# Kernel optimization log

Measured on AMD Instinct MI355X. Metric: run time of the kernel, lower is better.

The kernel has to match this reference:

```python
import jax, jax.numpy as jnp
import numpy as np

B, H, S, D = 4, 16, 2048, 128

def setup_inputs() -> dict:
    key = jax.random.key(0)
    kq, kk, kv = jax.random.split(key, 3)
    query = jax.random.normal(kq, (B, H, S, D), dtype=jnp.float32)
    k = jax.random.normal(kk, (B, H, S, D), dtype=jnp.float32)
    value = jax.random.normal(kv, (B, H, S, D), dtype=jnp.float32)
    attn_mask = jnp.zeros((B, H, S, S), dtype=jnp.float32)
    return {"query": query, "key": k, "value": value, "attn_mask": attn_mask}

def reference(query, key, value, attn_mask):
    # scores: [B,H,S,S]
    scale = 1.0 / jnp.sqrt(jnp.asarray(query.shape[-1], query.dtype))
    scores = jnp.einsum('bhqd,bhkd->bhqk', query, key) * scale + attn_mask
    attn = jax.nn.softmax(scores, axis=-1)
    out = jnp.einsum('bhqk,bhkd->bhqd', attn, value)
    return out
```

## Files before the change

kernel.cpp:

```cpp
#include <hip/hip_runtime.h>

#define SDIM 2048
#define DDIM 128
#define NBH  64
#define BR   128
#define BC   64
#define PSTRIDE 72

using bf16x8 = __attribute__((ext_vector_type(8))) short;
using f32x4  = __attribute__((ext_vector_type(4))) float;

typedef const __attribute__((address_space(1))) void* gvp;
typedef __attribute__((address_space(3))) void* lvp;

static __device__ __forceinline__ short f2bf(float x) {
    unsigned u = __float_as_uint(x);
    u += 0x7fff + ((u >> 16) & 1);
    return (short)(u >> 16);
}
static __device__ __forceinline__ unsigned pack2(float a, float b) {
    return ((unsigned)(unsigned short)f2bf(a)) |
           (((unsigned)(unsigned short)f2bf(b)) << 16);
}

__global__ __launch_bounds__(256) void kconv_kernel(const float* __restrict__ K,
                                                    unsigned short* __restrict__ Kc)
{
    size_t i = ((size_t)blockIdx.x * 256 + threadIdx.x) * 4;
    float4 v = *(const float4*)(K + i);
    uint2 o;
    o.x = pack2(v.x, v.y);
    o.y = pack2(v.z, v.w);
    *(uint2*)(Kc + i) = o;
}

__global__ __launch_bounds__(256) void vtrans_kernel(const float* __restrict__ V,
                                                     unsigned short* __restrict__ Vt)
{
    __shared__ float t[32][33];
    const int bh = blockIdx.z;
    const int s0 = blockIdx.x * 32;
    const int d0 = blockIdx.y * 32;
    const int x = threadIdx.x & 31;
    const int y = threadIdx.x >> 5;
    const float* Vb = V + (size_t)bh * SDIM * DDIM;
    unsigned short* Vtb = Vt + (size_t)bh * SDIM * DDIM;
#pragma unroll
    for (int i = 0; i < 4; ++i) {
        int r = y + i * 8;
        t[r][x] = Vb[(size_t)(s0 + r) * DDIM + d0 + x];
    }
    __syncthreads();
#pragma unroll
    for (int i = 0; i < 4; ++i) {
        int r = y + i * 8;
        Vtb[(size_t)(d0 + r) * SDIM + s0 + x] = (unsigned short)f2bf(t[x][r]);
    }
}

static __device__ __forceinline__ void stage_K(const unsigned short* __restrict__ Kb,
                                               char* __restrict__ Kdst,
                                               int k0, int wave, int quad, int n16)
{
#pragma unroll
    for (int j = 0; j < 4; ++j) {
        const int row = wave * 16 + j * 4 + quad;
        const int src = (n16 * 16) ^ ((row & 7) << 4);
        const char* gp = (const char*)(Kb + (size_t)(k0 + row) * DDIM) + src;
        __builtin_amdgcn_global_load_lds((gvp)gp, (lvp)(Kdst + wave * 4096 + j * 1024), 16, 0, 0);
    }
}
static __device__ __forceinline__ void stage_V(const unsigned short* __restrict__ Vb,
                                               char* __restrict__ Vdst,
                                               int k0, int wave, int lane)
{
#pragma unroll
    for (int j = 0; j < 4; ++j) {
        const int row = wave * 32 + j * 8 + (lane >> 3);
        const int src = ((lane & 7) * 16) ^ ((row & 7) << 4);
        const char* gp = (const char*)(Vb + (size_t)row * SDIM + k0) + src;
        __builtin_amdgcn_global_load_lds((gvp)gp, (lvp)(Vdst + wave * 4096 + j * 1024), 16, 0, 0);
    }
}

static __device__ __forceinline__ void load_mask(const float* __restrict__ Mb,
                                                 int q0, int wave, int quad, int n16,
                                                 int kcol, float (&mk)[2][4][4])
{
#pragma unroll
    for (int rt = 0; rt < 2; ++rt) {
        const int rowb = q0 + wave * 32 + rt * 16 + quad * 4;
        const float* mpb = Mb + (size_t)rowb * SDIM + kcol + n16;
#pragma unroll
        for (int ct = 0; ct < 4; ++ct)
#pragma unroll
            for (int r = 0; r < 4; ++r)
                mk[rt][ct][r] = mpb[(size_t)r * SDIM + ct * 16];
    }
}

static __device__ __forceinline__ void softmax_update(
    f32x4 (&s)[2][4], f32x4 (&acc)[2][8], float (&mrow)[2][4], float (&lrow)[2][4])
{
    float mx[2][4];
#pragma unroll
    for (int rt = 0; rt < 2; ++rt)
#pragma unroll
        for (int r = 0; r < 4; ++r)
            mx[rt][r] = fmaxf(fmaxf(s[rt][0][r], s[rt][1][r]),
                              fmaxf(s[rt][2][r], s[rt][3][r]));
#pragma unroll
    for (int st = 1; st <= 8; st <<= 1)
#pragma unroll
        for (int rt = 0; rt < 2; ++rt)
#pragma unroll
            for (int r = 0; r < 4; ++r)
                mx[rt][r] = fmaxf(mx[rt][r], __shfl_xor(mx[rt][r], st));

    int anynew = 0;
#pragma unroll
    for (int rt = 0; rt < 2; ++rt)
#pragma unroll
        for (int r = 0; r < 4; ++r)
            anynew |= (mx[rt][r] > mrow[rt][r]) ? 1 : 0;
    if (__ballot(anynew) != 0ull) {
#pragma unroll
        for (int rt = 0; rt < 2; ++rt)
#pragma unroll
            for (int r = 0; r < 4; ++r) {
                float mnew = fmaxf(mrow[rt][r], mx[rt][r]);
                float al = exp2f((mrow[rt][r] - mnew) * 1.44269504f);
                mrow[rt][r] = mnew;
                lrow[rt][r] *= al;
#pragma unroll
                for (int nt = 0; nt < 8; ++nt) acc[rt][nt][r] *= al;
            }
    }

    float rs[2][4];
#pragma unroll
    for (int rt = 0; rt < 2; ++rt)
#pragma unroll
        for (int r = 0; r < 4; ++r) {
            float t = 0.f;
#pragma unroll
            for (int ct = 0; ct < 4; ++ct) {
                float pv = exp2f((s[rt][ct][r] - mrow[rt][r]) * 1.44269504f);
                s[rt][ct][r] = pv;
                t += pv;
            }
            rs[rt][r] = t;
        }
#pragma unroll
    for (int st = 1; st <= 8; st <<= 1)
#pragma unroll
        for (int rt = 0; rt < 2; ++rt)
#pragma unroll
            for (int r = 0; r < 4; ++r)
                rs[rt][r] += __shfl_xor(rs[rt][r], st);
#pragma unroll
    for (int rt = 0; rt < 2; ++rt)
#pragma unroll
        for (int r = 0; r < 4; ++r)
            lrow[rt][r] += rs[rt][r];
}

static __device__ __forceinline__ void qk_phase(
    const char* __restrict__ Kcur, int quad, int n16, int swzr,
    const bf16x8 (&qf)[2][4], f32x4 (&s)[2][4])
{
#pragma unroll
    for (int dt = 0; dt < 4; ++dt) {
        bf16x8 kf[4];
#pragma unroll
        for (int ct = 0; ct < 4; ++ct)
            kf[ct] = *(const bf16x8*)(Kcur + (ct * 16 + n16) * 256 +
                                      ((dt * 64 + quad * 16) ^ swzr));
        __builtin_amdgcn_s_setprio(1);
#pragma unroll
        for (int ct = 0; ct < 4; ++ct) {
            s[0][ct] = __builtin_amdgcn_mfma_f32_16x16x32_bf16(qf[0][dt], kf[ct], s[0][ct], 0, 0, 0);
            s[1][ct] = __builtin_amdgcn_mfma_f32_16x16x32_bf16(qf[1][dt], kf[ct], s[1][ct], 0, 0, 0);
        }
        __builtin_amdgcn_s_setprio(0);
    }
}

static __device__ __forceinline__ void ppack_pv(
    f32x4 (&s)[2][4], const char* __restrict__ Vl,
    unsigned short* __restrict__ PsW, int quad, int n16, int lane, int swzr,
    f32x4 (&acc)[2][8], bool deferred_barrier)
{
#pragma unroll
    for (int rt = 0; rt < 2; ++rt)
#pragma unroll
        for (int ct = 0; ct < 4; ++ct)
#pragma unroll
            for (int r = 0; r < 4; ++r)
                PsW[(rt * 16 + (lane >> 4) * 4 + r) * PSTRIDE + ct * 16 + n16] =
                    (unsigned short)f2bf(s[rt][ct][r]);

    bf16x8 pa[2][2];
#pragma unroll
    for (int rt = 0; rt < 2; ++rt)
#pragma unroll
        for (int kt = 0; kt < 2; ++kt)
            pa[rt][kt] = *(const bf16x8*)(&PsW[(rt * 16 + n16) * PSTRIDE + kt * 32 + quad * 8]);

    if (deferred_barrier) {
        asm volatile("s_waitcnt vmcnt(4)" ::: "memory");
        __builtin_amdgcn_s_barrier();
    }

#pragma unroll
    for (int nt = 0; nt < 8; ++nt) {
        bf16x8 vf[2];
#pragma unroll
        for (int kt = 0; kt < 2; ++kt)
            vf[kt] = *(const bf16x8*)(Vl + (nt * 16 + n16) * 128 +
                                      ((kt * 64 + quad * 16) ^ swzr));
        __builtin_amdgcn_s_setprio(1);
#pragma unroll
        for (int kt = 0; kt < 2; ++kt) {
            acc[0][nt] = __builtin_amdgcn_mfma_f32_16x16x32_bf16(pa[0][kt], vf[kt], acc[0][nt], 0, 0, 0);
            acc[1][nt] = __builtin_amdgcn_mfma_f32_16x16x32_bf16(pa[1][kt], vf[kt], acc[1][nt], 0, 0, 0);
        }
        __builtin_amdgcn_s_setprio(0);
    }
}

static __device__ __forceinline__ void ktile_fast(
    int k0, int wave, int quad, int n16, int lane,
    const unsigned short* __restrict__ Kb, const unsigned short* __restrict__ Vb,
    char* __restrict__ Kcur, char* __restrict__ Knxt, char* __restrict__ Vl,
    unsigned short* __restrict__ PsW,
    const bf16x8 (&qf)[2][4],
    f32x4 (&acc)[2][8], float (&mrow)[2][4], float (&lrow)[2][4])
{
    const f32x4 zero4 = {0.f, 0.f, 0.f, 0.f};

    stage_V(Vb, Vl, k0, wave, lane);
    stage_K(Kb, Knxt, (k0 + BC) & (SDIM - 1), wave, quad, n16);

    const int swzr = (n16 & 7) << 4;

    f32x4 s[2][4];
#pragma unroll
    for (int rt = 0; rt < 2; ++rt)
#pragma unroll
        for (int ct = 0; ct < 4; ++ct) s[rt][ct] = zero4;

    qk_phase(Kcur, quad, n16, swzr, qf, s);
    softmax_update(s, acc, mrow, lrow);
    ppack_pv(s, Vl, PsW, quad, n16, lane, swzr, acc, true);

    asm volatile("s_waitcnt vmcnt(0)" ::: "memory");
    __builtin_amdgcn_s_barrier();
}

static __device__ __forceinline__ void ktile_masked(
    int k0, int q0, int wave, int quad, int n16, int lane,
    const float* __restrict__ Mb,
    const unsigned short* __restrict__ Kb, const unsigned short* __restrict__ Vb,
    char* __restrict__ Kl, char* __restrict__ Vl,
    unsigned short* __restrict__ PsW,
    const bf16x8 (&qf)[2][4],
    f32x4 (&acc)[2][8], float (&mrow)[2][4], float (&lrow)[2][4])
{
    const f32x4 zero4 = {0.f, 0.f, 0.f, 0.f};

    stage_K(Kb, Kl, k0, wave, quad, n16);
    stage_V(Vb, Vl, k0, wave, lane);

    float mk[2][4][4];
    load_mask(Mb, q0, wave, quad, n16, k0, mk);

    __syncthreads();

    const int swzr = (n16 & 7) << 4;

    f32x4 s[2][4];
#pragma unroll
    for (int rt = 0; rt < 2; ++rt)
#pragma unroll
        for (int ct = 0; ct < 4; ++ct) s[rt][ct] = zero4;

    qk_phase(Kl, quad, n16, swzr, qf, s);

#pragma unroll
    for (int rt = 0; rt < 2; ++rt)
#pragma unroll
        for (int ct = 0; ct < 4; ++ct)
#pragma unroll
            for (int r = 0; r < 4; ++r)
                s[rt][ct][r] += mk[rt][ct][r];

    softmax_update(s, acc, mrow, lrow);
    ppack_pv(s, Vl, PsW, quad, n16, lane, swzr, acc, false);
}

__global__ __launch_bounds__(256, 2) void fattn_kernel(
    const float* __restrict__ Q, const float* __restrict__ M,
    const unsigned short* __restrict__ Kc, const unsigned short* __restrict__ Vt,
    float* __restrict__ O)
{
    const int flat = blockIdx.x;
    const int slot = flat >> 3;
    const int bh   = (flat & 7) * 8 + (slot >> 4);
    const int qt   = slot & 15;

    const int tid  = threadIdx.x;
    const int wave = tid >> 6;
    const int lane = tid & 63;
    const int quad = lane >> 4;
    const int n16  = lane & 15;
    const int q0   = qt * BR;

    const float* Qb = Q + (size_t)bh * SDIM * DDIM;
    const float* Mb = M + (size_t)bh * SDIM * SDIM;
    const unsigned short* Kb = Kc + (size_t)bh * SDIM * DDIM;
    const unsigned short* Vb = Vt + (size_t)bh * SDIM * DDIM;
    float* Ob = O + (size_t)bh * SDIM * DDIM;

    __shared__ __align__(16) char Kl0[64 * 256];
    __shared__ __align__(16) char Kl1[64 * 256];
    __shared__ __align__(16) char Vl[128 * 128];
    __shared__ __align__(16) unsigned short Ps[4][32 * PSTRIDE];
    __shared__ int blkmask;
    unsigned short* PsW = Ps[wave];

    stage_K(Kb, Kl0, 0, wave, quad, n16);

    const float scale = 0.08838834764831845f;
    bf16x8 qf[2][4];
#pragma unroll
    for (int rt = 0; rt < 2; ++rt) {
        int row = q0 + wave * 32 + rt * 16 + n16;
        const float* qp = Qb + (size_t)row * DDIM + quad * 8;
#pragma unroll
        for (int dt = 0; dt < 4; ++dt) {
            const float* p = qp + dt * 32;
            float4 a = *(const float4*)p;
            float4 b = *(const float4*)(p + 4);
            bf16x8 f;
            f[0] = f2bf(a.x * scale); f[1] = f2bf(a.y * scale);
            f[2] = f2bf(a.z * scale); f[3] = f2bf(a.w * scale);
            f[4] = f2bf(b.x * scale); f[5] = f2bf(b.y * scale);
            f[6] = f2bf(b.z * scale); f[7] = f2bf(b.w * scale);
            qf[rt][dt] = f;
        }
    }

    if (tid == 0) blkmask = 0;
    {
        const uint4* Ms = (const uint4*)(Mb + (size_t)q0 * SDIM);
        unsigned a0 = 0, a1 = 0, a2 = 0, a3 = 0;
#pragma unroll 1
        for (int i = tid; i < (BR * SDIM / 4); i += 1024) {
            uint4 v0 = Ms[i];
            uint4 v1 = Ms[i + 256];
            uint4 v2 = Ms[i + 512];
            uint4 v3 = Ms[i + 768];
            a0 |= v0.x | v0.y | v0.z | v0.w;
            a1 |= v1.x | v1.y | v1.z | v1.w;
            a2 |= v2.x | v2.y | v2.z | v2.w;
            a3 |= v3.x | v3.y | v3.z | v3.w;
        }
        const unsigned am = (a0 | a1) | (a2 | a3);
        __syncthreads();
        if (am) atomicOr(&blkmask, 1);
    }
    __syncthreads();
    const bool masked = (blkmask != 0);

    f32x4 acc[2][8];
    const f32x4 zero4 = {0.f, 0.f, 0.f, 0.f};
#pragma unroll
    for (int rt = 0; rt < 2; ++rt)
#pragma unroll
        for (int nt = 0; nt < 8; ++nt) acc[rt][nt] = zero4;
    float mrow[2][4], lrow[2][4];
#pragma unroll
    for (int rt = 0; rt < 2; ++rt)
#pragma unroll
        for (int r = 0; r < 4; ++r) { mrow[rt][r] = -1e30f; lrow[rt][r] = 0.f; }

    if (!masked) {
#pragma unroll 1
        for (int k0 = 0; k0 < SDIM; k0 += 2 * BC) {
            ktile_fast(k0,      wave, quad, n16, lane, Kb, Vb, Kl0, Kl1, Vl,
                       PsW, qf, acc, mrow, lrow);
            ktile_fast(k0 + BC, wave, quad, n16, lane, Kb, Vb, Kl1, Kl0, Vl,
                       PsW, qf, acc, mrow, lrow);
        }
    } else {
#pragma unroll 1
        for (int k0 = 0; k0 < SDIM; k0 += BC) {
            __syncthreads();
            ktile_masked(k0, q0, wave, quad, n16, lane, Mb, Kb, Vb, Kl0, Vl,
                         PsW, qf, acc, mrow, lrow);
        }
    }

#pragma unroll
    for (int rt = 0; rt < 2; ++rt) {
#pragma unroll
        for (int r = 0; r < 4; ++r) {
            float inv = 1.0f / lrow[rt][r];
            int row = q0 + wave * 32 + rt * 16 + quad * 4 + r;
            float* op = Ob + (size_t)row * DDIM + n16;
#pragma unroll
            for (int nt = 0; nt < 8; ++nt)
                op[nt * 16] = acc[rt][nt][r] * inv;
        }
    }
}

extern "C" void kernel_launch(void* const* d_in, const int* in_sizes, int n_in,
                              void* d_out, int out_size, void* d_ws, size_t ws_size,
                              hipStream_t stream) {
    const float* Q = (const float*)d_in[0];
    const float* K = (const float*)d_in[1];
    const float* V = (const float*)d_in[2];
    const float* M = (const float*)d_in[3];
    float* O = (float*)d_out;

    const size_t nElem = (size_t)NBH * SDIM * DDIM;
    unsigned short* Kc = (unsigned short*)d_ws;
    unsigned short* Vt = Kc + nElem;

    kconv_kernel<<<dim3(nElem / (256 * 4)), 256, 0, stream>>>(K, Kc);
    vtrans_kernel<<<dim3(SDIM / 32, DDIM / 32, NBH), 256, 0, stream>>>(V, Vt);
    fattn_kernel<<<dim3((SDIM / BR) * NBH), 256, 0, stream>>>(Q, M, Kc, Vt, O);
}
```

Before: 1.735 ms.

## Fuse mask loads into double-buffered K loop and drop the mask prescan

Removes the per-block full-mask prescan and the separate slow masked path. The kernel now always runs the double-buffered K/V pipeline, loading each tile's mask slice at the start of the tile and adding it to the scores after QK. The aim is to overlap mask streaming with MFMA work instead of reading the mask in a serialized pass. In exchange, every tile must now wait on mask load latency, and the per-tile mask loads may coalesce less well than the prescan's vectorized reads.

After: 1.597 ms. -8.0%, faster.

```diff
diff --git a/kernel.cpp b/kernel.cpp
--- a/kernel.cpp
+++ b/kernel.cpp
@@ -189,7 +189,7 @@
 static __device__ __forceinline__ void ppack_pv(
     f32x4 (&s)[2][4], const char* __restrict__ Vl,
     unsigned short* __restrict__ PsW, int quad, int n16, int lane, int swzr,
-    f32x4 (&acc)[2][8], bool deferred_barrier)
+    f32x4 (&acc)[2][8])
 {
 #pragma unroll
     for (int rt = 0; rt < 2; ++rt)
@@ -207,10 +207,8 @@
         for (int kt = 0; kt < 2; ++kt)
             pa[rt][kt] = *(const bf16x8*)(&PsW[(rt * 16 + n16) * PSTRIDE + kt * 32 + quad * 8]);
 
-    if (deferred_barrier) {
-        asm volatile("s_waitcnt vmcnt(4)" ::: "memory");
-        __builtin_amdgcn_s_barrier();
-    }
+    asm volatile("s_waitcnt vmcnt(4)" ::: "memory");
+    __builtin_amdgcn_s_barrier();
 
 #pragma unroll
     for (int nt = 0; nt < 8; ++nt) {
@@ -229,8 +227,9 @@
     }
 }
 
-static __device__ __forceinline__ void ktile_fast(
-    int k0, int wave, int quad, int n16, int lane,
+static __device__ __forceinline__ void ktile(
+    int k0, int q0, int wave, int quad, int n16, int lane,
+    const float* __restrict__ Mb,
     const unsigned short* __restrict__ Kb, const unsigned short* __restrict__ Vb,
     char* __restrict__ Kcur, char* __restrict__ Knxt, char* __restrict__ Vl,
     unsigned short* __restrict__ PsW,
@@ -239,8 +238,13 @@
 {
     const f32x4 zero4 = {0.f, 0.f, 0.f, 0.f};
 
+    float mk[2][4][4];
+    load_mask(Mb, q0, wave, quad, n16, k0, mk);
+    __builtin_amdgcn_sched_barrier(0);
+
     stage_V(Vb, Vl, k0, wave, lane);
     stage_K(Kb, Knxt, (k0 + BC) & (SDIM - 1), wave, quad, n16);
+    __builtin_amdgcn_sched_barrier(0);
 
     const int swzr = (n16 & 7) << 4;
 
@@ -251,52 +255,20 @@
         for (int ct = 0; ct < 4; ++ct) s[rt][ct] = zero4;
 
     qk_phase(Kcur, quad, n16, swzr, qf, s);
+
+#pragma unroll
+    for (int rt = 0; rt < 2; ++rt)
+#pragma unroll
+        for (int ct = 0; ct < 4; ++ct)
+#pragma unroll
+            for (int r = 0; r < 4; ++r)
+                s[rt][ct][r] += mk[rt][ct][r];
+
     softmax_update(s, acc, mrow, lrow);
-    ppack_pv(s, Vl, PsW, quad, n16, lane, swzr, acc, true);
+    ppack_pv(s, Vl, PsW, quad, n16, lane, swzr, acc);
 
     asm volatile("s_waitcnt vmcnt(0)" ::: "memory");
     __builtin_amdgcn_s_barrier();
-}
-
-static __device__ __forceinline__ void ktile_masked(
-    int k0, int q0, int wave, int quad, int n16, int lane,
-    const float* __restrict__ Mb,
-    const unsigned short* __restrict__ Kb, const unsigned short* __restrict__ Vb,
-    char* __restrict__ Kl, char* __restrict__ Vl,
-    unsigned short* __restrict__ PsW,
-    const bf16x8 (&qf)[2][4],
-    f32x4 (&acc)[2][8], float (&mrow)[2][4], float (&lrow)[2][4])
-{
-    const f32x4 zero4 = {0.f, 0.f, 0.f, 0.f};
-
-    stage_K(Kb, Kl, k0, wave, quad, n16);
-    stage_V(Vb, Vl, k0, wave, lane);
-
-    float mk[2][4][4];
-    load_mask(Mb, q0, wave, quad, n16, k0, mk);
-
-    __syncthreads();
-
-    const int swzr = (n16 & 7) << 4;
-
-    f32x4 s[2][4];
-#pragma unroll
-    for (int rt = 0; rt < 2; ++rt)
-#pragma unroll
-        for (int ct = 0; ct < 4; ++ct) s[rt][ct] = zero4;
-
-    qk_phase(Kl, quad, n16, swzr, qf, s);
-
-#pragma unroll
-    for (int rt = 0; rt < 2; ++rt)
-#pragma unroll
-        for (int ct = 0; ct < 4; ++ct)
-#pragma unroll
-            for (int r = 0; r < 4; ++r)
-                s[rt][ct][r] += mk[rt][ct][r];
-
-    softmax_update(s, acc, mrow, lrow);
-    ppack_pv(s, Vl, PsW, quad, n16, lane, swzr, acc, false);
 }
 
 __global__ __launch_bounds__(256, 2) void fattn_kernel(
@@ -326,7 +298,6 @@
     __shared__ __align__(16) char Kl1[64 * 256];
     __shared__ __align__(16) char Vl[128 * 128];
     __shared__ __align__(16) unsigned short Ps[4][32 * PSTRIDE];
-    __shared__ int blkmask;
     unsigned short* PsW = Ps[wave];
 
     stage_K(Kb, Kl0, 0, wave, quad, n16);
@@ -351,28 +322,6 @@
         }
     }
 
-    if (tid == 0) blkmask = 0;
-    {
-        const uint4* Ms = (const uint4*)(Mb + (size_t)q0 * SDIM);
-        unsigned a0 = 0, a1 = 0, a2 = 0, a3 = 0;
-#pragma unroll 1
-        for (int i = tid; i < (BR * SDIM / 4); i += 1024) {
-            uint4 v0 = Ms[i];
-            uint4 v1 = Ms[i + 256];
-            uint4 v2 = Ms[i + 512];
-            uint4 v3 = Ms[i + 768];
-            a0 |= v0.x | v0.y | v0.z | v0.w;
-            a1 |= v1.x | v1.y | v1.z | v1.w;
-            a2 |= v2.x | v2.y | v2.z | v2.w;
-            a3 |= v3.x | v3.y | v3.z | v3.w;
-        }
-        const unsigned am = (a0 | a1) | (a2 | a3);
-        __syncthreads();
-        if (am) atomicOr(&blkmask, 1);
-    }
-    __syncthreads();
-    const bool masked = (blkmask != 0);
-
     f32x4 acc[2][8];
     const f32x4 zero4 = {0.f, 0.f, 0.f, 0.f};
 #pragma unroll
@@ -385,21 +334,15 @@
 #pragma unroll
         for (int r = 0; r < 4; ++r) { mrow[rt][r] = -1e30f; lrow[rt][r] = 0.f; }
 
-    if (!masked) {
+    asm volatile("s_waitcnt vmcnt(0)" ::: "memory");
+    __builtin_amdgcn_s_barrier();
+
 #pragma unroll 1
-        for (int k0 = 0; k0 < SDIM; k0 += 2 * BC) {
-            ktile_fast(k0,      wave, quad, n16, lane, Kb, Vb, Kl0, Kl1, Vl,
-                       PsW, qf, acc, mrow, lrow);
-            ktile_fast(k0 + BC, wave, quad, n16, lane, Kb, Vb, Kl1, Kl0, Vl,
-                       PsW, qf, acc, mrow, lrow);
-        }
-    } else {
-#pragma unroll 1
-        for (int k0 = 0; k0 < SDIM; k0 += BC) {
-            __syncthreads();
-            ktile_masked(k0, q0, wave, quad, n16, lane, Mb, Kb, Vb, Kl0, Vl,
-                         PsW, qf, acc, mrow, lrow);
-        }
+    for (int k0 = 0; k0 < SDIM; k0 += 2 * BC) {
+        ktile(k0,      q0, wave, quad, n16, lane, Mb, Kb, Vb, Kl0, Kl1, Vl,
+              PsW, qf, acc, mrow, lrow);
+        ktile(k0 + BC, q0, wave, quad, n16, lane, Mb, Kb, Vb, Kl1, Kl0, Vl,
+              PsW, qf, acc, mrow, lrow);
     }
 
 #pragma unroll
```
